# Performance work log

Hardware: AMD Instinct MI355X
Metric: run time of the kernel (lower is better)

## Reference

```python
import jax, jax.numpy as jnp
import numpy as np

N = 30000        # nodes
E = 480000       # edges
IN = 256         # input feature dim
D = 32           # num_hidden per head
H = 4            # heads for layers 0,1
C = 47           # num_classes (final layer, 1 head)
NEG_SLOPE = 0.2


def setup_inputs() -> dict:
    key = jax.random.key(0)
    ks = jax.random.split(key, 16)
    def glorot(k, shape):
        fan = sum(shape)
        return jax.random.normal(k, shape, jnp.float32) * jnp.sqrt(2.0 / fan)
    inp = {
        "x": jax.random.normal(ks[0], (N, IN), jnp.float32),
        # layer 0: IN -> H*D, no residual
        "W0": glorot(ks[1], (IN, H * D)),
        "al0": glorot(ks[2], (H, D)),
        "ar0": glorot(ks[3], (H, D)),
        # layer 1: H*D -> H*D, residual fc
        "W1": glorot(ks[4], (H * D, H * D)),
        "resW1": glorot(ks[5], (H * D, H * D)),
        "al1": glorot(ks[6], (H, D)),
        "ar1": glorot(ks[7], (H, D)),
        # final layer: H*D -> 1*C, residual fc
        "W2": glorot(ks[8], (H * D, 1 * C)),
        "resW2": glorot(ks[9], (H * D, 1 * C)),
        "al2": glorot(ks[10], (1, C)),
        "ar2": glorot(ks[11], (1, C)),
        "src": jax.random.randint(ks[12], (E,), 0, N, jnp.int32),
        "dst": jax.random.randint(ks[13], (E,), 0, N, jnp.int32),
    }
    return inp


def gat_layer(h, W, al, ar, src, dst, heads, d, resW=None, act=None):
    # h: [N, F_in]; W: [F_in, heads*d]; al/ar: [heads, d]
    n = h.shape[0]
    feat = (h @ W).reshape(n, heads, d)                 # [N, H, D]
    el = (feat * al).sum(-1)                            # [N, H]
    er = (feat * ar).sum(-1)                            # [N, H]
    e = jax.nn.leaky_relu(el[src] + er[dst], NEG_SLOPE)  # [E, H]
    # edge softmax over incoming edges of each dst node (numerically stable)
    emax = jax.ops.segment_max(e, dst, num_segments=n)  # [N, H]
    emax = jnp.where(jnp.isfinite(emax), emax, 0.0)     # guard empty segments
    w = jnp.exp(e - emax[dst])                          # [E, H]
    wsum = jax.ops.segment_sum(w, dst, num_segments=n)  # [N, H]
    a = w / jnp.maximum(wsum[dst], 1e-9)                # [E, H]
    msg = feat[src] * a[:, :, None]                     # [E, H, D]
    rst = jax.ops.segment_sum(msg, dst, num_segments=n)  # [N, H, D]
    if resW is not None:
        rst = rst + (h @ resW).reshape(n, heads, d)
    if act is not None:
        rst = act(rst)
    return rst, e


def reference(x, W0, al0, ar0, W1, resW1, al1, ar1, W2, resW2, al2, ar2, src, dst):
    act = jax.nn.elu
    # layer 0 (no residual, no in-conv activation), then flatten + activation
    h, e0 = gat_layer(x, W0, al0, ar0, src, dst, H, D)
    h = act(h.reshape(N, H * D))
    # layer 1 (residual, in-conv activation), then flatten + activation
    h, e1 = gat_layer(h, W1, al1, ar1, src, dst, H, D, resW=resW1, act=act)
    h = act(h.reshape(N, H * D))
    # final layer (residual, no activation), mean over heads
    h, e2 = gat_layer(h, W2, al2, ar2, src, dst, 1, C, resW=resW2)
    logits = h.mean(axis=1)                             # [N, C]
    return (logits, e0, e1, e2)
```

## Files before the change

### kernel.cpp

```cpp
#include <hip/hip_runtime.h>
#include <hip/hip_bf16.h>
#include <math.h>

#define NN 30000
#define NE 480000
#define FIN 256
#define DH 32
#define NH 4
#define NC 47
#define NODE_BLKS 7500
#define EDGE_BLKS 1875
#define SCAN_CHUNK 1000

typedef __attribute__((ext_vector_type(8))) short frag_ab;
typedef __attribute__((ext_vector_type(4))) float f32x4;
typedef __hip_bfloat16 bf16;

static inline size_t align256(size_t x) { return (x + 255) & ~(size_t)255; }

__device__ __forceinline__ short f2bf(float f) {
    union { float f; unsigned u; } c; c.f = f;
    unsigned r = (c.u + 0x7FFFu + ((c.u >> 16) & 1u)) >> 16;
    return (short)r;
}
__device__ __forceinline__ float b2f(unsigned short u) {
    union { unsigned u; float f; } c; c.u = (unsigned)u << 16; return c.f;
}
__device__ __forceinline__ float expw(float v) {
    return __expf((v >= 0.f) ? v : 0.2f * v);
}
__device__ __forceinline__ float lrelu(float v) {
    return (v >= 0.f) ? v : 0.2f * v;
}

__global__ void count_k(const int* __restrict__ dst, int* __restrict__ cnt, int E) {
    int e = blockIdx.x * blockDim.x + threadIdx.x;
    if (e < E) atomicAdd(&cnt[dst[e]], 1);
}

__global__ __launch_bounds__(1024) void scanA(const int* __restrict__ cnt,
                                              int* __restrict__ offs,
                                              int* __restrict__ bsum) {
    __shared__ int warp_sums[16];
    const int lane = threadIdx.x & 63;
    const int wid = threadIdx.x >> 6;
    const int g = blockIdx.x * SCAN_CHUNK + threadIdx.x;
    const bool valid = (threadIdx.x < SCAN_CHUNK) && (g < NN);
    int v = valid ? cnt[g] : 0;
    int x = v;
    #pragma unroll
    for (int off = 1; off < 64; off <<= 1) {
        int y = __shfl_up(x, off);
        if (lane >= off) x += y;
    }
    if (lane == 63) warp_sums[wid] = x;
    __syncthreads();
    if (wid == 0) {
        int ws = (lane < 16) ? warp_sums[lane] : 0;
        #pragma unroll
        for (int off = 1; off < 16; off <<= 1) {
            int y = __shfl_up(ws, off);
            if (lane >= off) ws += y;
        }
        if (lane < 16) warp_sums[lane] = ws;
    }
    __syncthreads();
    const int wbase = (wid > 0) ? warp_sums[wid - 1] : 0;
    const int incl = x + wbase;
    if (valid) offs[g] = incl - v;
    if (threadIdx.x == 1023) bsum[blockIdx.x] = incl;
}

__global__ __launch_bounds__(256) void scanB(const int* __restrict__ bsum,
                                             int* __restrict__ offs,
                                             int* __restrict__ cursor) {
    __shared__ int bases[31];
    if (threadIdx.x == 0) {
        int acc = 0;
        for (int j = 0; j < 30; ++j) { bases[j] = acc; acc += bsum[j]; }
        bases[30] = acc;
    }
    __syncthreads();
    const int i = blockIdx.x * 256 + threadIdx.x;
    if (i < NN) {
        const int o = offs[i] + bases[i / SCAN_CHUNK];
        offs[i] = o;
        cursor[i] = o;
    }
    if (i == 0) offs[NN] = bases[30];
}

__global__ void fill_k(const int* __restrict__ dst, const int* __restrict__ src,
                       int* __restrict__ cursor, int* __restrict__ srcs, int E) {
    int e = blockIdx.x * blockDim.x + threadIdx.x;
    if (e < E) {
        int p = atomicAdd(&cursor[dst[e]], 1);
        srcs[p] = src[e];
    }
}

__global__ void prep_w_all(const float* __restrict__ W0, const float* __restrict__ W1,
                           const float* __restrict__ rW1, const float* __restrict__ W2,
                           const float* __restrict__ rW2,
                           const float* __restrict__ al0, const float* __restrict__ ar0,
                           const float* __restrict__ al1, const float* __restrict__ ar1,
                           const float* __restrict__ al2, const float* __restrict__ ar2,
                           bf16* __restrict__ W0t, bf16* __restrict__ W1t,
                           bf16* __restrict__ rW1t, bf16* __restrict__ W2t,
                           bf16* __restrict__ rW2t, int* __restrict__ cursor) {
    if (blockIdx.y == 5) {
        int i = blockIdx.x * 256 + threadIdx.x;
        if (i < NN) cursor[i] = 0;
        return;
    }
    const float *W, *al, *ar; bf16* Wt; int K, M, rows, H, D;
    switch (blockIdx.y) {
        case 0: W = W0;  Wt = W0t;  K = 256; M = 128; rows = 144; H = 4; D = 32; al = al0; ar = ar0; break;
        case 1: W = W1;  Wt = W1t;  K = 128; M = 128; rows = 144; H = 4; D = 32; al = al1; ar = ar1; break;
        case 2: W = rW1; Wt = rW1t; K = 128; M = 128; rows = 128; H = 0; D = 0;  al = nullptr; ar = nullptr; break;
        case 3: W = W2;  Wt = W2t;  K = 128; M = 47;  rows = 64;  H = 1; D = 47; al = al2; ar = ar2; break;
        default: W = rW2; Wt = rW2t; K = 128; M = 47; rows = 48;  H = 0; D = 0;  al = nullptr; ar = nullptr; break;
    }
    int i = blockIdx.x * 256 + threadIdx.x;
    if (i >= rows * K) return;
    int row = i / K, k = i - row * K;
    float v = 0.f;
    if (row < M) {
        v = W[(long)k * M + row];
    } else if (H > 0 && row < M + 2 * H) {
        int idx = row - M;
        int h = (idx < H) ? idx : idx - H;
        const float* a = (idx < H) ? al : ar;
        float s = 0.f;
        for (int d = 0; d < D; ++d) s += W[(long)k * M + h * D + d] * a[h * D + d];
        v = s;
    }
    Wt[i] = __float2bfloat16(v);
}

template <bool A_F32, int NT1, int NT2, int HH>
__global__ __launch_bounds__(256) void gemm_mfma(
    const void* __restrict__ Av, const bf16* __restrict__ B1t,
    const bf16* __restrict__ B2t,
    bf16* __restrict__ C1b, float* __restrict__ el, float* __restrict__ er,
    float* __restrict__ C2, int N, int K, int M) {
    constexpr int LP = 56;
    __shared__ bf16 As[64][LP];
    __shared__ bf16 Bs1[NT1 * 16][LP];
    __shared__ bf16 Bs2[(NT2 > 0) ? NT2 * 16 : 1][LP];

    const int tid = threadIdx.x;
    const int lane = tid & 63;
    const int wid = tid >> 6;
    const int row0 = blockIdx.x * 64;
    const int l15 = lane & 15;
    const int kq = lane >> 4;

    f32x4 acc1[NT1], acc2[(NT2 > 0) ? NT2 : 1];
    #pragma unroll
    for (int t = 0; t < NT1; ++t) acc1[t] = (f32x4){0.f, 0.f, 0.f, 0.f};
    if constexpr (NT2 > 0) {
        #pragma unroll
        for (int t = 0; t < NT2; ++t) acc2[t] = (f32x4){0.f, 0.f, 0.f, 0.f};
    }

    for (int k0 = 0; k0 < K; k0 += 32) {
        {
            const int r = tid >> 2, kk = (tid & 3) * 8;
            const int gr = row0 + r;
            if constexpr (A_F32) {
                const float* A = (const float*)Av;
                short tmp[8];
                if (gr < N) {
                    const float4 v0 = *(const float4*)&A[(long)gr * K + k0 + kk];
                    const float4 v1 = *(const float4*)&A[(long)gr * K + k0 + kk + 4];
                    tmp[0] = f2bf(v0.x); tmp[1] = f2bf(v0.y); tmp[2] = f2bf(v0.z); tmp[3] = f2bf(v0.w);
                    tmp[4] = f2bf(v1.x); tmp[5] = f2bf(v1.y); tmp[6] = f2bf(v1.z); tmp[7] = f2bf(v1.w);
                } else {
                    #pragma unroll
                    for (int j = 0; j < 8; ++j) tmp[j] = 0;
                }
                *(frag_ab*)&As[r][kk] = *(const frag_ab*)tmp;
            } else {
                const bf16* A = (const bf16*)Av;
                frag_ab v = {0, 0, 0, 0, 0, 0, 0, 0};
                if (gr < N) v = *(const frag_ab*)&A[(long)gr * K + k0 + kk];
                *(frag_ab*)&As[r][kk] = v;
            }
        }
        for (int i = tid; i < NT1 * 64; i += 256) {
            const int c = i >> 2, kk = (i & 3) * 8;
            *(frag_ab*)&Bs1[c][kk] = *(const frag_ab*)&B1t[(long)c * K + k0 + kk];
        }
        if constexpr (NT2 > 0) {
            for (int i = tid; i < NT2 * 64; i += 256) {
                const int c = i >> 2, kk = (i & 3) * 8;
                *(frag_ab*)&Bs2[c][kk] = *(const frag_ab*)&B2t[(long)c * K + k0 + kk];
            }
        }
        __syncthreads();

        const frag_ab a = *(const frag_ab*)&As[wid * 16 + l15][kq * 8];
        #pragma unroll
        for (int t = 0; t < NT1; ++t) {
            const frag_ab b = *(const frag_ab*)&Bs1[t * 16 + l15][kq * 8];
            acc1[t] = __builtin_amdgcn_mfma_f32_16x16x32_bf16(a, b, acc1[t], 0, 0, 0);
        }
        if constexpr (NT2 > 0) {
            #pragma unroll
            for (int t = 0; t < NT2; ++t) {
                const frag_ab b = *(const frag_ab*)&Bs2[t * 16 + l15][kq * 8];
                acc2[t] = __builtin_amdgcn_mfma_f32_16x16x32_bf16(a, b, acc2[t], 0, 0, 0);
            }
        }
        __syncthreads();
    }

    const int r0 = row0 + wid * 16 + kq * 4;
    #pragma unroll
    for (int t = 0; t < NT1; ++t) {
        const int c = t * 16 + l15;
        #pragma unroll
        for (int reg = 0; reg < 4; ++reg) {
            const int r = r0 + reg;
            if (r >= N) continue;
            const float v = acc1[t][reg];
            if (c < M) {
                C1b[(long)r * M + c] = __float2bfloat16(v);
            } else if (c < M + HH) {
                el[(long)r * HH + (c - M)] = v;
            } else if (c < M + 2 * HH) {
                er[(long)r * HH + (c - M - HH)] = v;
            }
        }
    }
    if constexpr (NT2 > 0) {
        #pragma unroll
        for (int t = 0; t < NT2; ++t) {
            const int c = t * 16 + l15;
            if (c >= M) continue;
            #pragma unroll
            for (int reg = 0; reg < 4; ++reg) {
                const int r = r0 + reg;
                if (r < N) C2[(long)r * M + c] = acc2[t][reg];
            }
        }
    }
}

template <int NELU, bool HAS_RES>
__global__ __launch_bounds__(256) void node_agg4(
    const bf16* __restrict__ featb, const float4* __restrict__ el4,
    const float4* __restrict__ er4, float4* __restrict__ es4,
    const int* __restrict__ offs, const int* __restrict__ srcs,
    const float* __restrict__ res, bf16* __restrict__ out) {
    __shared__ float4 sc[4][64];
    const int node = (int)((blockIdx.x * blockDim.x + threadIdx.x) >> 6);
    const int lane = threadIdx.x & 63;
    const int wid = threadIdx.x >> 6;
    const int beg = offs[node], end = offs[node + 1];
    const float4 ern = er4[node];

    float4 s4 = make_float4(0.f, 0.f, 0.f, 0.f);
    for (int i = beg + lane; i < end; i += 64) {
        const float4 elv = el4[srcs[i]];
        float4 t;
        t.x = expw(elv.x + ern.x); t.y = expw(elv.y + ern.y);
        t.z = expw(elv.z + ern.z); t.w = expw(elv.w + ern.w);
        s4.x += t.x; s4.y += t.y; s4.z += t.z; s4.w += t.w;
        const int idx = i - beg;
        if (idx < 64) sc[wid][idx] = t;
        else es4[i] = t;
    }
    #pragma unroll
    for (int off = 32; off > 0; off >>= 1) {
        s4.x += __shfl_xor(s4.x, off);
        s4.y += __shfl_xor(s4.y, off);
        s4.z += __shfl_xor(s4.z, off);
        s4.w += __shfl_xor(s4.w, off);
    }
    __syncthreads();

    const int q = lane >> 4;
    const int l15 = lane & 15;
    const int fi = l15 * 8;
    const int h = l15 >> 2;
    const float sh = (h == 0) ? s4.x : (h == 1) ? s4.y : (h == 2) ? s4.z : s4.w;
    const float inv = 1.f / fmaxf(sh, 1e-9f);
    const float* esf = (const float*)es4;
    const float* scf = (const float*)sc[wid];

    float a[8] = {0.f, 0.f, 0.f, 0.f, 0.f, 0.f, 0.f, 0.f};
    int i = beg + q;
    for (; i + 4 < end; i += 8) {
        const int iB = i + 4;
        const int idxA = i - beg, idxB = iB - beg;
        const int snA = srcs[i], snB = srcs[iB];
        const float wA = (idxA < 64) ? scf[idxA * 4 + h] : esf[i * 4 + h];
        const float wB = (idxB < 64) ? scf[idxB * 4 + h] : esf[iB * 4 + h];
        const frag_ab fA = *(const frag_ab*)(featb + (long)snA * 128 + fi);
        const frag_ab fB = *(const frag_ab*)(featb + (long)snB * 128 + fi);
        #pragma unroll
        for (int j = 0; j < 8; ++j)
            a[j] += wA * b2f((unsigned short)fA[j]) + wB * b2f((unsigned short)fB[j]);
    }
    for (; i < end; i += 4) {
        const int idx = i - beg;
        const int sn = srcs[i];
        const float w = (idx < 64) ? scf[idx * 4 + h] : esf[i * 4 + h];
        const frag_ab f = *(const frag_ab*)(featb + (long)sn * 128 + fi);
        #pragma unroll
        for (int j = 0; j < 8; ++j) a[j] += w * b2f((unsigned short)f[j]);
    }
    #pragma unroll
    for (int j = 0; j < 8; ++j) {
        a[j] += __shfl_xor(a[j], 16);
        a[j] += __shfl_xor(a[j], 32);
    }

    if (lane < 16) {
        float v[8];
        #pragma unroll
        for (int j = 0; j < 8; ++j) v[j] = a[j] * inv;
        if constexpr (HAS_RES) {
            const float4 r0 = *(const float4*)(res + (long)node * 128 + fi);
            const float4 r1 = *(const float4*)(res + (long)node * 128 + fi + 4);
            v[0] += r0.x; v[1] += r0.y; v[2] += r0.z; v[3] += r0.w;
            v[4] += r1.x; v[5] += r1.y; v[6] += r1.z; v[7] += r1.w;
        }
        #pragma unroll
        for (int t = 0; t < NELU; ++t)
            #pragma unroll
            for (int j = 0; j < 8; ++j)
                v[j] = (v[j] > 0.f) ? v[j] : expm1f(v[j]);
        frag_ab o;
        #pragma unroll
        for (int j = 0; j < 8; ++j) o[j] = f2bf(v[j]);
        *(frag_ab*)(out + (long)node * 128 + fi) = o;
    }
}

__global__ __launch_bounds__(256) void final_k(
    const bf16* __restrict__ featb, const float* __restrict__ el2s,
    const float* __restrict__ er2s, float* __restrict__ es1,
    const int* __restrict__ offs, const int* __restrict__ srcs,
    const float* __restrict__ res, float* __restrict__ logits,
    const float4* __restrict__ el0, const float4* __restrict__ er0,
    const float4* __restrict__ el1, const float4* __restrict__ er1,
    const int* __restrict__ src, const int* __restrict__ dst,
    float* __restrict__ e0, float* __restrict__ e1, float* __restrict__ e2) {
    __shared__ float sc1[4][64];
    if (blockIdx.x < NODE_BLKS) {
        const int node = (int)((blockIdx.x * blockDim.x + threadIdx.x) >> 6);
        const int lane = threadIdx.x & 63;
        const int wid = threadIdx.x >> 6;
        const int beg = offs[node], end = offs[node + 1];
        const float ern = er2s[node];

        float s = 0.f;
        for (int i = beg + lane; i < end; i += 64) {
            const float t = expw(el2s[srcs[i]] + ern);
            s += t;
            const int idx = i - beg;
            if (idx < 64) sc1[wid][idx] = t;
            else es1[i] = t;
        }
        #pragma unroll
        for (int off = 32; off > 0; off >>= 1) s += __shfl_xor(s, off);
        const float inv = 1.f / fmaxf(s, 1e-9f);
        __syncthreads();

        const bool active = lane < NC;
        float acc = 0.f;
        int i = beg;
        for (; i + 8 <= end; i += 8) {
            const int d0 = i - beg;
            int sn[8]; float w[8];
            #pragma unroll
            for (int k = 0; k < 8; ++k) {
                sn[k] = srcs[i + k];
                w[k] = (d0 + k < 64) ? sc1[wid][d0 + k] : es1[i + k];
            }
            if (active) {
                #pragma unroll
                for (int k = 0; k < 8; ++k)
                    acc += w[k] * __bfloat162float(featb[(long)sn[k] * NC + lane]);
            }
        }
        for (; i < end; ++i) {
            const int idx = i - beg;
            const float w = (idx < 64) ? sc1[wid][idx] : es1[i];
            if (active) acc += w * __bfloat162float(featb[(long)srcs[i] * NC + lane]);
        }
        if (active) {
            logits[(long)node * NC + lane] = acc * inv + res[(long)node * NC + lane];
        }
    } else {
        const int e = (blockIdx.x - NODE_BLKS) * 256 + threadIdx.x;
        const int s = src[e], d = dst[e];
        const float4 a0 = el0[s], b0 = er0[d];
        float4 v0;
        v0.x = lrelu(a0.x + b0.x); v0.y = lrelu(a0.y + b0.y);
        v0.z = lrelu(a0.z + b0.z); v0.w = lrelu(a0.w + b0.w);
        *reinterpret_cast<float4*>(e0 + e * 4) = v0;
        const float4 a1 = el1[s], b1 = er1[d];
        float4 v1;
        v1.x = lrelu(a1.x + b1.x); v1.y = lrelu(a1.y + b1.y);
        v1.z = lrelu(a1.z + b1.z); v1.w = lrelu(a1.w + b1.w);
        *reinterpret_cast<float4*>(e1 + e * 4) = v1;
        e2[e] = lrelu(el2s[s] + er2s[d]);
    }
}

extern "C" void kernel_launch(void* const* d_in, const int* in_sizes, int n_in,
                              void* d_out, int out_size, void* d_ws, size_t ws_size,
                              hipStream_t stream) {
    const float* x     = (const float*)d_in[0];
    const float* W0    = (const float*)d_in[1];
    const float* al0   = (const float*)d_in[2];
    const float* ar0   = (const float*)d_in[3];
    const float* W1    = (const float*)d_in[4];
    const float* resW1 = (const float*)d_in[5];
    const float* al1   = (const float*)d_in[6];
    const float* ar1   = (const float*)d_in[7];
    const float* W2    = (const float*)d_in[8];
    const float* resW2 = (const float*)d_in[9];
    const float* al2   = (const float*)d_in[10];
    const float* ar2   = (const float*)d_in[11];
    const int*   src   = (const int*)d_in[12];
    const int*   dst   = (const int*)d_in[13];

    float* out    = (float*)d_out;
    float* logits = out;
    float* e0     = out + (long)NN * NC;
    float* e1     = e0 + (long)NE * NH;
    float* e2     = e1 + (long)NE * NH;

    char* p = (char*)d_ws;
    int* offs   = (int*)p; p += align256(sizeof(int) * (NN + 1));
    int* cursor = (int*)p; p += align256(sizeof(int) * NN);
    int* bsum   = (int*)p; p += align256(sizeof(int) * 32);
    int* srcs   = (int*)p; p += align256(sizeof(int) * NE);
    float* el0b = (float*)p; p += align256(sizeof(float) * NN * NH);
    float* er0b = (float*)p; p += align256(sizeof(float) * NN * NH);
    float* el1b = (float*)p; p += align256(sizeof(float) * NN * NH);
    float* er1b = (float*)p; p += align256(sizeof(float) * NN * NH);
    float* el2b = (float*)p; p += align256(sizeof(float) * NN);
    float* er2b = (float*)p; p += align256(sizeof(float) * NN);
    float* es   = (float*)p; p += align256(sizeof(float) * (long)NE * NH);
    float* resb = (float*)p; p += align256(sizeof(float) * (long)NN * 128);
    bf16* featb = (bf16*)p; p += align256(sizeof(bf16) * (long)NN * 128);
    bf16* hb    = (bf16*)p; p += align256(sizeof(bf16) * (long)NN * 128);
    bf16* W0t   = (bf16*)p; p += align256(sizeof(bf16) * 144 * 256);
    bf16* W1t   = (bf16*)p; p += align256(sizeof(bf16) * 144 * 128);
    bf16* rW1t  = (bf16*)p; p += align256(sizeof(bf16) * 128 * 128);
    bf16* W2t   = (bf16*)p; p += align256(sizeof(bf16) * 64 * 128);
    bf16* rW2t  = (bf16*)p; p += align256(sizeof(bf16) * 48 * 128);

    prep_w_all<<<dim3(144, 6), 256, 0, stream>>>(W0, W1, resW1, W2, resW2,
                                                 al0, ar0, al1, ar1, al2, ar2,
                                                 W0t, W1t, rW1t, W2t, rW2t, cursor);

    count_k<<<EDGE_BLKS, 256, 0, stream>>>(dst, cursor, NE);
    scanA<<<30, 1024, 0, stream>>>(cursor, offs, bsum);
    scanB<<<(NN + 255) / 256, 256, 0, stream>>>(bsum, offs, cursor);
    fill_k<<<EDGE_BLKS, 256, 0, stream>>>(dst, src, cursor, srcs, NE);

    const int gemmBlocks = (NN + 63) / 64;

    gemm_mfma<true, 9, 0, NH><<<gemmBlocks, 256, 0, stream>>>(
        x, W0t, nullptr, featb, el0b, er0b, nullptr, NN, FIN, 128);
    node_agg4<1, false><<<NODE_BLKS, 256, 0, stream>>>(
        featb, (const float4*)el0b, (const float4*)er0b, (float4*)es, offs, srcs, nullptr, hb);

    gemm_mfma<false, 9, 8, NH><<<gemmBlocks, 256, 0, stream>>>(
        hb, W1t, rW1t, featb, el1b, er1b, resb, NN, 128, 128);
    node_agg4<2, true><<<NODE_BLKS, 256, 0, stream>>>(
        featb, (const float4*)el1b, (const float4*)er1b, (float4*)es, offs, srcs, resb, hb);

    gemm_mfma<false, 4, 3, 1><<<gemmBlocks, 256, 0, stream>>>(
        hb, W2t, rW2t, featb, el2b, er2b, resb, NN, 128, NC);
    final_k<<<NODE_BLKS + EDGE_BLKS, 256, 0, stream>>>(
        featb, el2b, er2b, es, offs, srcs, resb, logits,
        (const float4*)el0b, (const float4*)er0b,
        (const float4*)el1b, (const float4*)er1b,
        src, dst, e0, e1, e2);
}
```

Measured before the change: 203.9 us.

## Fuse CSR build steps and edge-score writes into gemm and prep kernels

Merges the degree-count pass into the weight-prep kernel (cursor zeroed by memset), folds the per-chunk scan into extra blocks of the first GEMM launch, and moves the layer-0 and layer-1 edge-score outputs into tail blocks of the later GEMM launches. Fewer kernel launches and better overlap of small memory-bound work with the GEMMs are the goal. The final kernel now writes only e2. In exchange the prep grid grows to 1875 blocks per y-slice, most of which exit early, and the GEMM kernels take many more parameters.

```diff
diff --git a/kernel.cpp b/kernel.cpp
--- a/kernel.cpp
+++ b/kernel.cpp
@@ -10,7 +10,8 @@
 #define NC 47
 #define NODE_BLKS 7500
 #define EDGE_BLKS 1875
-#define SCAN_CHUNK 1000
+#define SCAN_CHUNK 1024
+#define NCHUNKS 30
 
 typedef __attribute__((ext_vector_type(8))) short frag_ab;
 typedef __attribute__((ext_vector_type(4))) float f32x4;
@@ -33,73 +34,7 @@
     return (v >= 0.f) ? v : 0.2f * v;
 }
 
-__global__ void count_k(const int* __restrict__ dst, int* __restrict__ cnt, int E) {
-    int e = blockIdx.x * blockDim.x + threadIdx.x;
-    if (e < E) atomicAdd(&cnt[dst[e]], 1);
-}
-
-__global__ __launch_bounds__(1024) void scanA(const int* __restrict__ cnt,
-                                              int* __restrict__ offs,
-                                              int* __restrict__ bsum) {
-    __shared__ int warp_sums[16];
-    const int lane = threadIdx.x & 63;
-    const int wid = threadIdx.x >> 6;
-    const int g = blockIdx.x * SCAN_CHUNK + threadIdx.x;
-    const bool valid = (threadIdx.x < SCAN_CHUNK) && (g < NN);
-    int v = valid ? cnt[g] : 0;
-    int x = v;
-    #pragma unroll
-    for (int off = 1; off < 64; off <<= 1) {
-        int y = __shfl_up(x, off);
-        if (lane >= off) x += y;
-    }
-    if (lane == 63) warp_sums[wid] = x;
-    __syncthreads();
-    if (wid == 0) {
-        int ws = (lane < 16) ? warp_sums[lane] : 0;
-        #pragma unroll
-        for (int off = 1; off < 16; off <<= 1) {
-            int y = __shfl_up(ws, off);
-            if (lane >= off) ws += y;
-        }
-        if (lane < 16) warp_sums[lane] = ws;
-    }
-    __syncthreads();
-    const int wbase = (wid > 0) ? warp_sums[wid - 1] : 0;
-    const int incl = x + wbase;
-    if (valid) offs[g] = incl - v;
-    if (threadIdx.x == 1023) bsum[blockIdx.x] = incl;
-}
-
-__global__ __launch_bounds__(256) void scanB(const int* __restrict__ bsum,
-                                             int* __restrict__ offs,
-                                             int* __restrict__ cursor) {
-    __shared__ int bases[31];
-    if (threadIdx.x == 0) {
-        int acc = 0;
-        for (int j = 0; j < 30; ++j) { bases[j] = acc; acc += bsum[j]; }
-        bases[30] = acc;
-    }
-    __syncthreads();
-    const int i = blockIdx.x * 256 + threadIdx.x;
-    if (i < NN) {
-        const int o = offs[i] + bases[i / SCAN_CHUNK];
-        offs[i] = o;
-        cursor[i] = o;
-    }
-    if (i == 0) offs[NN] = bases[30];
-}
-
-__global__ void fill_k(const int* __restrict__ dst, const int* __restrict__ src,
-                       int* __restrict__ cursor, int* __restrict__ srcs, int E) {
-    int e = blockIdx.x * blockDim.x + threadIdx.x;
-    if (e < E) {
-        int p = atomicAdd(&cursor[dst[e]], 1);
-        srcs[p] = src[e];
-    }
-}
-
-__global__ void prep_w_all(const float* __restrict__ W0, const float* __restrict__ W1,
+__global__ void prep_count(const float* __restrict__ W0, const float* __restrict__ W1,
                            const float* __restrict__ rW1, const float* __restrict__ W2,
                            const float* __restrict__ rW2,
                            const float* __restrict__ al0, const float* __restrict__ ar0,
@@ -107,10 +42,11 @@
                            const float* __restrict__ al2, const float* __restrict__ ar2,
                            bf16* __restrict__ W0t, bf16* __restrict__ W1t,
                            bf16* __restrict__ rW1t, bf16* __restrict__ W2t,
-                           bf16* __restrict__ rW2t, int* __restrict__ cursor) {
+                           bf16* __restrict__ rW2t,
+                           const int* __restrict__ dst, int* __restrict__ cursor) {
     if (blockIdx.y == 5) {
-        int i = blockIdx.x * 256 + threadIdx.x;
-        if (i < NN) cursor[i] = 0;
+        int e = blockIdx.x * 256 + threadIdx.x;
+        if (e < NE) atomicAdd(&cursor[dst[e]], 1);
         return;
     }
     const float *W, *al, *ar; bf16* Wt; int K, M, rows, H, D;
@@ -138,18 +74,96 @@
     Wt[i] = __float2bfloat16(v);
 }
 
-template <bool A_F32, int NT1, int NT2, int HH>
+__global__ __launch_bounds__(256) void scanB(const int* __restrict__ bsum,
+                                             int* __restrict__ offs,
+                                             int* __restrict__ cursor) {
+    __shared__ int bases[NCHUNKS + 1];
+    if (threadIdx.x == 0) {
+        int acc = 0;
+        for (int j = 0; j < NCHUNKS; ++j) { bases[j] = acc; acc += bsum[j]; }
+        bases[NCHUNKS] = acc;
+    }
+    __syncthreads();
+    const int i = blockIdx.x * 256 + threadIdx.x;
+    if (i < NN) {
+        const int o = offs[i] + bases[i >> 10];
+        offs[i] = o;
+        cursor[i] = o;
+    }
+    if (i == 0) offs[NN] = bases[NCHUNKS];
+}
+
+__global__ void fill_k(const int* __restrict__ dst, const int* __restrict__ src,
+                       int* __restrict__ cursor, int* __restrict__ srcs, int E) {
+    int e = blockIdx.x * blockDim.x + threadIdx.x;
+    if (e < E) {
+        int p = atomicAdd(&cursor[dst[e]], 1);
+        srcs[p] = src[e];
+    }
+}
+
+template <bool A_F32, int NT1, int NT2, int HH, int TAIL>
 __global__ __launch_bounds__(256) void gemm_mfma(
     const void* __restrict__ Av, const bf16* __restrict__ B1t,
     const bf16* __restrict__ B2t,
     bf16* __restrict__ C1b, float* __restrict__ el, float* __restrict__ er,
-    float* __restrict__ C2, int N, int K, int M) {
+    float* __restrict__ C2, int N, int K, int M, int nGemmBlocks,
+    const int* __restrict__ t_cnt, int* __restrict__ t_offs, int* __restrict__ t_bsum,
+    const float4* __restrict__ pel, const float4* __restrict__ per,
+    const int* __restrict__ src, const int* __restrict__ dst,
+    float* __restrict__ eout) {
     constexpr int LP = 56;
     __shared__ bf16 As[64][LP];
     __shared__ bf16 Bs1[NT1 * 16][LP];
     __shared__ bf16 Bs2[(NT2 > 0) ? NT2 * 16 : 1][LP];
+    __shared__ int ws4[4];
 
     const int tid = threadIdx.x;
+
+    if constexpr (TAIL == 1) {
+        if (blockIdx.x >= nGemmBlocks) {
+            const int chunk = blockIdx.x - nGemmBlocks;
+            const int lane = tid & 63;
+            const int wid = tid >> 6;
+            const int g = chunk * SCAN_CHUNK + tid * 4;
+            const int a0 = (g + 0 < NN) ? t_cnt[g + 0] : 0;
+            const int a1 = (g + 1 < NN) ? t_cnt[g + 1] : 0;
+            const int a2 = (g + 2 < NN) ? t_cnt[g + 2] : 0;
+            const int a3 = (g + 3 < NN) ? t_cnt[g + 3] : 0;
+            const int lsum = a0 + a1 + a2 + a3;
+            int x = lsum;
+            #pragma unroll
+            for (int off = 1; off < 64; off <<= 1) {
+                int y = __shfl_up(x, off);
+                if (lane >= off) x += y;
+            }
+            if (lane == 63) ws4[wid] = x;
+            __syncthreads();
+            int wbase = 0;
+            #pragma unroll
+            for (int j = 0; j < 4; ++j) if (j < wid) wbase += ws4[j];
+            const int excl = wbase + x - lsum;
+            if (g + 0 < NN) t_offs[g + 0] = excl;
+            if (g + 1 < NN) t_offs[g + 1] = excl + a0;
+            if (g + 2 < NN) t_offs[g + 2] = excl + a0 + a1;
+            if (g + 3 < NN) t_offs[g + 3] = excl + a0 + a1 + a2;
+            if (tid == 0) t_bsum[chunk] = ws4[0] + ws4[1] + ws4[2] + ws4[3];
+            return;
+        }
+    }
+    if constexpr (TAIL == 2) {
+        if (blockIdx.x >= nGemmBlocks) {
+            const int e = (blockIdx.x - nGemmBlocks) * 256 + tid;
+            const int s = src[e], d = dst[e];
+            const float4 a = pel[s], b = per[d];
+            float4 v;
+            v.x = lrelu(a.x + b.x); v.y = lrelu(a.y + b.y);
+            v.z = lrelu(a.z + b.z); v.w = lrelu(a.w + b.w);
+            *reinterpret_cast<float4*>(eout + e * 4) = v;
+            return;
+        }
+    }
+
     const int lane = tid & 63;
     const int wid = tid >> 6;
     const int row0 = blockIdx.x * 64;
@@ -345,10 +359,8 @@
     const float* __restrict__ er2s, float* __restrict__ es1,
     const int* __restrict__ offs, const int* __restrict__ srcs,
     const float* __restrict__ res, float* __restrict__ logits,
-    const float4* __restrict__ el0, const float4* __restrict__ er0,
-    const float4* __restrict__ el1, const float4* __restrict__ er1,
     const int* __restrict__ src, const int* __restrict__ dst,
-    float* __restrict__ e0, float* __restrict__ e1, float* __restrict__ e2) {
+    float* __restrict__ e2) {
     __shared__ float sc1[4][64];
     if (blockIdx.x < NODE_BLKS) {
         const int node = (int)((blockIdx.x * blockDim.x + threadIdx.x) >> 6);
@@ -397,18 +409,7 @@
         }
     } else {
         const int e = (blockIdx.x - NODE_BLKS) * 256 + threadIdx.x;
-        const int s = src[e], d = dst[e];
-        const float4 a0 = el0[s], b0 = er0[d];
-        float4 v0;
-        v0.x = lrelu(a0.x + b0.x); v0.y = lrelu(a0.y + b0.y);
-        v0.z = lrelu(a0.z + b0.z); v0.w = lrelu(a0.w + b0.w);
-        *reinterpret_cast<float4*>(e0 + e * 4) = v0;
-        const float4 a1 = el1[s], b1 = er1[d];
-        float4 v1;
-        v1.x = lrelu(a1.x + b1.x); v1.y = lrelu(a1.y + b1.y);
-        v1.z = lrelu(a1.z + b1.z); v1.w = lrelu(a1.w + b1.w);
-        *reinterpret_cast<float4*>(e1 + e * 4) = v1;
-        e2[e] = lrelu(el2s[s] + er2s[d]);
+        e2[e] = lrelu(el2s[src[e]] + er2s[dst[e]]);
     }
 }
 
@@ -457,32 +458,36 @@
     bf16* W2t   = (bf16*)p; p += align256(sizeof(bf16) * 64 * 128);
     bf16* rW2t  = (bf16*)p; p += align256(sizeof(bf16) * 48 * 128);
 
-    prep_w_all<<<dim3(144, 6), 256, 0, stream>>>(W0, W1, resW1, W2, resW2,
-                                                 al0, ar0, al1, ar1, al2, ar2,
-                                                 W0t, W1t, rW1t, W2t, rW2t, cursor);
-
-    count_k<<<EDGE_BLKS, 256, 0, stream>>>(dst, cursor, NE);
-    scanA<<<30, 1024, 0, stream>>>(cursor, offs, bsum);
+    const int gemmBlocks = (NN + 63) / 64;
+
+    hipMemsetAsync(cursor, 0, sizeof(int) * NN, stream);
+    prep_count<<<dim3(EDGE_BLKS, 6), 256, 0, stream>>>(
+        W0, W1, resW1, W2, resW2, al0, ar0, al1, ar1, al2, ar2,
+        W0t, W1t, rW1t, W2t, rW2t, dst, cursor);
+
+    gemm_mfma<true, 9, 0, NH, 1><<<gemmBlocks + NCHUNKS, 256, 0, stream>>>(
+        x, W0t, nullptr, featb, el0b, er0b, nullptr, NN, FIN, 128, gemmBlocks,
+        cursor, offs, bsum, nullptr, nullptr, nullptr, nullptr, nullptr);
+
     scanB<<<(NN + 255) / 256, 256, 0, stream>>>(bsum, offs, cursor);
     fill_k<<<EDGE_BLKS, 256, 0, stream>>>(dst, src, cursor, srcs, NE);
 
-    const int gemmBlocks = (NN + 63) / 64;
-
-    gemm_mfma<true, 9, 0, NH><<<gemmBlocks, 256, 0, stream>>>(
-        x, W0t, nullptr, featb, el0b, er0b, nullptr, NN, FIN, 128);
     node_agg4<1, false><<<NODE_BLKS, 256, 0, stream>>>(
         featb, (const float4*)el0b, (const float4*)er0b, (float4*)es, offs, srcs, nullptr, hb);
 
-    gemm_mfma<false, 9, 8, NH><<<gemmBlocks, 256, 0, stream>>>(
-        hb, W1t, rW1t, featb, el1b, er1b, resb, NN, 128, 128);
+    gemm_mfma<false, 9, 8, NH, 2><<<gemmBlocks + EDGE_BLKS, 256, 0, stream>>>(
+        hb, W1t, rW1t, featb, el1b, er1b, resb, NN, 128, 128, gemmBlocks,
+        nullptr, nullptr, nullptr,
+        (const float4*)el0b, (const float4*)er0b, src, dst, e0);
+
     node_agg4<2, true><<<NODE_BLKS, 256, 0, stream>>>(
         featb, (const float4*)el1b, (const float4*)er1b, (float4*)es, offs, srcs, resb, hb);
 
-    gemm_mfma<false, 4, 3, 1><<<gemmBlocks, 256, 0, stream>>>(
-        hb, W2t, rW2t, featb, el2b, er2b, resb, NN, 128, NC);
+    gemm_mfma<false, 4, 3, 1, 2><<<gemmBlocks + EDGE_BLKS, 256, 0, stream>>>(
+        hb, W2t, rW2t, featb, el2b, er2b, resb, NN, 128, NC, gemmBlocks,
+        nullptr, nullptr, nullptr,
+        (const float4*)el1b, (const float4*)er1b, src, dst, e1);
+
     final_k<<<NODE_BLKS + EDGE_BLKS, 256, 0, stream>>>(
-        featb, el2b, er2b, es, offs, srcs, resb, logits,
-        (const float4*)el0b, (const float4*)er0b,
-        (const float4*)el1b, (const float4*)er1b,
-        src, dst, e0, e1, e2);
-}
+        featb, el2b, er2b, es, offs, srcs, resb, logits, src, dst, e2);
+}
```

Measured after the change: 201.7 us. Within noise of the previous version (-1.1%).
